# Performance work log

Measured on AMD Instinct MI355X. Metric: run time of the kernel, lower is better.

The kernel has to match this reference:

```python
import jax, jax.numpy as jnp
import numpy as np

N = 100000      # nodes
E = 400000      # edges per relation
R = 4           # relations
D_IN, D_HID, D_OUT = 256, 256, 128


def setup_inputs() -> dict:
    key = jax.random.key(0)
    ks = jax.random.split(key, 6)
    x = jax.random.normal(ks[0], (N, D_IN), jnp.float32)
    src = jax.random.randint(ks[1], (R, E), 0, N)
    dst = jax.random.randint(ks[2], (R, E), 0, N)
    # glorot-ish init for per-relation GraphConv weights
    W1 = jax.random.normal(ks[3], (R, D_IN, D_HID), jnp.float32) * (1.0 / np.sqrt(D_IN))
    b1 = jnp.zeros((R, D_HID), jnp.float32)
    W2 = jax.random.normal(ks[4], (R, D_HID, D_OUT), jnp.float32) * (1.0 / np.sqrt(D_HID))
    b2 = jnp.zeros((R, D_OUT), jnp.float32)
    return {"x": x, "src": src, "dst": dst, "W1": W1, "b1": b1, "W2": W2, "b2": b2}


def _rel_graphconv(x, src, dst, W, b):
    """DGL GraphConv with norm='both': D_dst^{-1/2} A D_src^{-1/2} X W + b.
    x: [N, din]; src/dst: [E]; W: [din, dout]; b: [dout]."""
    n = x.shape[0]
    xw = x @ W                                                   # [N, dout]
    ones = jnp.ones(src.shape, jnp.float32)
    out_deg = jnp.maximum(jax.ops.segment_sum(ones, src, num_segments=n), 1.0)
    in_deg = jnp.maximum(jax.ops.segment_sum(ones, dst, num_segments=n), 1.0)
    msg = xw[src] * (out_deg[src] ** -0.5)[:, None]              # [E, dout] gather + src-norm
    agg = jax.ops.segment_sum(msg, dst, num_segments=n)          # [N, dout] scatter-add
    return agg * (in_deg ** -0.5)[:, None] + b


def _hetero_layer(x, src, dst, W, b):
    # HeteroGraphConv(aggregate='sum'): run GraphConv per relation, sum results.
    conv = jax.vmap(_rel_graphconv, in_axes=(None, 0, 0, 0, 0))
    return jnp.sum(conv(x, src, dst, W, b), axis=0)              # [N, dout]


def reference(x, src, dst, W1, b1, W2, b2):
    h = jax.nn.relu(_hetero_layer(x, src, dst, W1, b1))
    return _hetero_layer(h, src, dst, W2, b2)
```

## Files before the change

### kernel.cpp

```cpp
#include <hip/hip_runtime.h>


#define RELS 4
#define DIN 256
#define DHID 256
#define DOUT 128

typedef short short8 __attribute__((ext_vector_type(8)));
typedef unsigned short ushort8 __attribute__((ext_vector_type(8)));
typedef float f32x4 __attribute__((ext_vector_type(4)));


__device__ __forceinline__ unsigned short f2bf(float f) {
    unsigned int u = __float_as_uint(f);
    u += 0x7FFFu + ((u >> 16) & 1u);
    return (unsigned short)(u >> 16);
}
__device__ __forceinline__ float bf2f(unsigned short u) {
    return __uint_as_float(((unsigned int)u) << 16);
}


__global__ void hist_kernel(const int* __restrict__ src, const int* __restrict__ dst,
                            int* __restrict__ cnt_src, int* __restrict__ cnt_dst,
                            int E, int N) {
    int i = blockIdx.x * blockDim.x + threadIdx.x;
    if (i >= RELS * E) return;
    int r = i / E;
    atomicAdd(cnt_src + (size_t)r * N + src[i], 1);
    atomicAdd(cnt_dst + (size_t)r * N + dst[i], 1);
}

__global__ void norm_kernel(const int* __restrict__ cnt, float* __restrict__ nrm, long n) {
    long i = blockIdx.x * (long)blockDim.x + threadIdx.x;
    if (i >= n) return;
    nrm[i] = rsqrtf(fmaxf((float)cnt[i], 1.0f));
}

__global__ void scan_block(const int* __restrict__ counts, int* __restrict__ out,
                           int* __restrict__ blk_sums, int n) {
    __shared__ int sh[256];
    int i = blockIdx.x * 256 + threadIdx.x;
    int v = (i < n) ? counts[i] : 0;
    sh[threadIdx.x] = v;
    __syncthreads();
#pragma unroll
    for (int off = 1; off < 256; off <<= 1) {
        int t = (threadIdx.x >= off) ? sh[threadIdx.x - off] : 0;
        __syncthreads();
        sh[threadIdx.x] += t;
        __syncthreads();
    }
    if (i < n) out[i] = sh[threadIdx.x] - v;
    if (threadIdx.x == 255) blk_sums[blockIdx.x] = sh[255];
}

__global__ void scan_sums(int* __restrict__ bs, int nb) {
    __shared__ int sh[256];
    __shared__ int carry;
    if (threadIdx.x == 0) carry = 0;
    __syncthreads();
    for (int base = 0; base < nb; base += 256) {
        int i = base + threadIdx.x;
        int v = (i < nb) ? bs[i] : 0;
        sh[threadIdx.x] = v;
        __syncthreads();
#pragma unroll
        for (int off = 1; off < 256; off <<= 1) {
            int t = (threadIdx.x >= off) ? sh[threadIdx.x - off] : 0;
            __syncthreads();
            sh[threadIdx.x] += t;
            __syncthreads();
        }
        if (i < nb) bs[i] = sh[threadIdx.x] - v + carry;
        int tot = sh[255];
        __syncthreads();
        if (threadIdx.x == 255) carry += tot;
        __syncthreads();
    }
}

__global__ void scan_add(int* __restrict__ out, int* __restrict__ cursor,
                         const int* __restrict__ blk_sums, int n, int total) {
    int i = blockIdx.x * 256 + threadIdx.x;
    if (i < n) {
        int v = out[i] + blk_sums[blockIdx.x];
        out[i] = v;
        cursor[i] = v;
    }
    if (i == n - 1) out[n] = total;
}

__global__ void fill_kernel(const int* __restrict__ src, const int* __restrict__ dst,
                            const float* __restrict__ nsrc,
                            int* __restrict__ cursor, int2* __restrict__ e_pack,
                            int E, int N) {
    int i = blockIdx.x * blockDim.x + threadIdx.x;
    if (i >= RELS * E) return;
    int r = i / E;
    int s = src[i];
    int pos = atomicAdd(cursor + (size_t)r * N + dst[i], 1);
    e_pack[pos] = make_int2(s, __float_as_int(nsrc[(size_t)r * N + s]));
}


__global__ void prep_fused(const float* __restrict__ x, const float* __restrict__ W1,
                           const float* __restrict__ W2, const float* __restrict__ b1,
                           const float* __restrict__ b2,
                           unsigned short* __restrict__ x_bf, unsigned short* __restrict__ w1t,
                           unsigned short* __restrict__ w2t,
                           float* __restrict__ b1s, float* __restrict__ b2s, long n8x) {
    const int T1 = RELS * DIN * DHID;
    const int T2 = RELS * DHID * DOUT;
    long i = blockIdx.x * (long)blockDim.x + threadIdx.x;
    if (i < n8x) {
        const float4* ip = (const float4*)(x + i * 8);
        float4 v0 = ip[0], v1 = ip[1];
        ushort4 o0 = make_ushort4(f2bf(v0.x), f2bf(v0.y), f2bf(v0.z), f2bf(v0.w));
        ushort4 o1 = make_ushort4(f2bf(v1.x), f2bf(v1.y), f2bf(v1.z), f2bf(v1.w));
        ushort4* op = (ushort4*)(x_bf + i * 8);
        op[0] = o0; op[1] = o1;
    } else if (i < n8x + T1) {
        int j = (int)(i - n8x);
        int r = j / (DIN * DHID);
        int rem = j - r * (DIN * DHID);
        int k = rem / DHID, n = rem - k * DHID;
        w1t[(size_t)n * (RELS * DIN) + r * DIN + k] = f2bf(W1[j]);
    } else if (i < n8x + T1 + T2) {
        int j = (int)(i - n8x - T1);
        int r = j / (DHID * DOUT);
        int rem = j - r * (DHID * DOUT);
        int k = rem / DOUT, n = rem - k * DOUT;
        w2t[((size_t)r * DOUT + n) * DHID + k] = f2bf(W2[j]);
    } else if (i < n8x + T1 + T2 + DHID + DOUT) {
        int c = (int)(i - n8x - T1 - T2);
        if (c < DHID) {
            b1s[c] = b1[c] + b1[DHID + c] + b1[2 * DHID + c] + b1[3 * DHID + c];
        } else {
            int cc = c - DHID;
            b2s[cc] = b2[cc] + b2[DOUT + cc] + b2[2 * DOUT + cc] + b2[3 * DOUT + cc];
        }
    }
}


__device__ __forceinline__ void gload_lds16(const void* g, void* l) {
    __builtin_amdgcn_global_load_lds(
        (const __attribute__((address_space(1))) void*)g,
        (__attribute__((address_space(3))) void*)l, 16, 0, 0);
}

template <int MODE>
__global__ __launch_bounds__(256) void gemm_bf16(
    const unsigned short* __restrict__ A, const unsigned short* __restrict__ Bt,
    unsigned short* __restrict__ C, int M, int Nout, int K,
    const float* __restrict__ scale_or_bias, int cols_per_rel, int Nnodes) {
    __shared__ unsigned short smA[128 * 32];
    __shared__ unsigned short smB[128 * 32];
    const int tid = threadIdx.x;
    const int lane = tid & 63;
    const int wid = tid >> 6;
    const int wr = wid >> 1, wc = wid & 1;
    const int brow = blockIdx.x * 128, bcol = blockIdx.y * 128;

    f32x4 acc[4][4] = {};

    const int s = lane >> 4;
    const int rl = lane & 15;

    for (int k0 = 0; k0 < K; k0 += 32) {
#pragma unroll
        for (int q = 0; q < 2; ++q) {
            int c = q * 256 + tid;
            int cl = c ^ ((c >> 3) & 3);
            int row = cl >> 2, slot = cl & 3;
            int ga = brow + row; ga = ga < M ? ga : M - 1;
            size_t ldsoff = (size_t)(q * 256 + (tid & ~63)) * 16;
            gload_lds16(A + (size_t)ga * K + k0 + slot * 8, (char*)smA + ldsoff);
            gload_lds16(Bt + (size_t)(bcol + row) * K + k0 + slot * 8, (char*)smB + ldsoff);
        }
        asm volatile("s_waitcnt vmcnt(0)" ::: "memory");
        __syncthreads();

        short8 a[4], b[4];
#pragma unroll
        for (int i = 0; i < 4; ++i) {
            int r = wr * 64 + i * 16 + rl;
            int ch = r * 4 + (s ^ ((r >> 1) & 3));
            a[i] = *(const short8*)((const char*)smA + ch * 16);
        }
#pragma unroll
        for (int j = 0; j < 4; ++j) {
            int r = wc * 64 + j * 16 + rl;
            int ch = r * 4 + (s ^ ((r >> 1) & 3));
            b[j] = *(const short8*)((const char*)smB + ch * 16);
        }
#pragma unroll
        for (int i = 0; i < 4; ++i)
#pragma unroll
            for (int j = 0; j < 4; ++j)
                acc[i][j] = __builtin_amdgcn_mfma_f32_16x16x32_bf16(a[i], b[j], acc[i][j], 0, 0, 0);
        __syncthreads();
    }

    const int rq = lane >> 4;
    if (MODE == 0) {
        const int relid = bcol / cols_per_rel;
        const float* nsr = scale_or_bias + (size_t)relid * Nnodes;
#pragma unroll
        for (int i = 0; i < 4; ++i) {
            int rbase = brow + wr * 64 + i * 16 + rq * 4;
            float sc[4];
#pragma unroll
            for (int t = 0; t < 4; ++t) {
                int row = rbase + t;
                sc[t] = (row < M) ? nsr[row] : 0.f;
            }
#pragma unroll
            for (int j = 0; j < 4; ++j) {
                int col = bcol + wc * 64 + j * 16 + rl;
#pragma unroll
                for (int t = 0; t < 4; ++t) {
                    int row = rbase + t;
                    if (row < M) C[(size_t)row * Nout + col] = f2bf(acc[i][j][t] * sc[t]);
                }
            }
        }
    } else {
#pragma unroll
        for (int i = 0; i < 4; ++i) {
            int rbase = brow + wr * 64 + i * 16 + rq * 4;
#pragma unroll
            for (int j = 0; j < 4; ++j) {
                int col = bcol + wc * 64 + j * 16 + rl;
                float bb = scale_or_bias[col];
#pragma unroll
                for (int t = 0; t < 4; ++t) {
                    int row = rbase + t;
                    if (row < M) C[(size_t)row * Nout + col] = f2bf(fmaxf(acc[i][j][t] + bb, 0.f));
                }
            }
        }
    }
}


__global__ void gather1_agg(const unsigned short* __restrict__ x_bf,
                            const int* __restrict__ rp, const int2* __restrict__ e_pack,
                            const float* __restrict__ ndst,
                            unsigned short* __restrict__ agg4, int N) {
    long w = (blockIdx.x * (long)blockDim.x + threadIdx.x) >> 6;
    int d = (int)(w >> 2);
    if (d >= N) return;
    int r = (int)(w & 3);
    int lane = threadIdx.x & 63;
    int h = lane >> 5, l = lane & 31;
    int beg = rp[(size_t)r * N + d], end = rp[(size_t)r * N + d + 1];
    float acc0[8] = {}, acc1[8] = {};
    int e = beg + h;
    for (; e + 2 < end; e += 4) {
        int2 p0 = e_pack[e];
        int2 p1 = e_pack[e + 2];
        ushort8 v0 = *(const ushort8*)(x_bf + (size_t)p0.x * DIN + l * 8);
        ushort8 v1 = *(const ushort8*)(x_bf + (size_t)p1.x * DIN + l * 8);
        float ns0 = __int_as_float(p0.y);
        float ns1 = __int_as_float(p1.y);
#pragma unroll
        for (int j = 0; j < 8; ++j) {
            acc0[j] += ns0 * bf2f(v0[j]);
            acc1[j] += ns1 * bf2f(v1[j]);
        }
    }
    if (e < end) {
        int2 p0 = e_pack[e];
        ushort8 v0 = *(const ushort8*)(x_bf + (size_t)p0.x * DIN + l * 8);
        float ns0 = __int_as_float(p0.y);
#pragma unroll
        for (int j = 0; j < 8; ++j) acc0[j] += ns0 * bf2f(v0[j]);
    }
    float nd = ndst[(size_t)r * N + d];
    ushort8 o;
#pragma unroll
    for (int j = 0; j < 8; ++j) {
        float v = acc0[j] + acc1[j];
        v += __shfl_xor(v, 32);
        o[j] = f2bf(nd * v);
    }
    if (h == 0)
        __builtin_nontemporal_store(o, (ushort8*)(agg4 + (size_t)d * (RELS * DIN) + r * DIN + l * 8));
}

__global__ void gather2_fused(const unsigned short* __restrict__ hw4,
                              const int* __restrict__ rp, const int2* __restrict__ e_pack,
                              const float* __restrict__ ndst, const float* __restrict__ b2s,
                              float* __restrict__ out, int N) {
    int wid = (int)((blockIdx.x * (long)blockDim.x + threadIdx.x) >> 6);
    if (wid >= N) return;
    int lane = threadIdx.x & 63;
    int h = lane >> 5, l = lane & 31;
    float oacc[4] = {};
#pragma unroll
    for (int r = 0; r < RELS; ++r) {
        int beg = rp[(size_t)r * N + wid], end = rp[(size_t)r * N + wid + 1];
        float acc0[4] = {}, acc1[4] = {};
        int e = beg + h;
        for (; e + 2 < end; e += 4) {
            int s0 = e_pack[e].x;
            int s1 = e_pack[e + 2].x;
            ushort4 v0 = *(const ushort4*)(hw4 + (size_t)s0 * (RELS * DOUT) + r * DOUT + l * 4);
            ushort4 v1 = *(const ushort4*)(hw4 + (size_t)s1 * (RELS * DOUT) + r * DOUT + l * 4);
            acc0[0] += bf2f(v0.x); acc0[1] += bf2f(v0.y); acc0[2] += bf2f(v0.z); acc0[3] += bf2f(v0.w);
            acc1[0] += bf2f(v1.x); acc1[1] += bf2f(v1.y); acc1[2] += bf2f(v1.z); acc1[3] += bf2f(v1.w);
        }
        if (e < end) {
            int s0 = e_pack[e].x;
            ushort4 v0 = *(const ushort4*)(hw4 + (size_t)s0 * (RELS * DOUT) + r * DOUT + l * 4);
            acc0[0] += bf2f(v0.x); acc0[1] += bf2f(v0.y); acc0[2] += bf2f(v0.z); acc0[3] += bf2f(v0.w);
        }
        float nd = ndst[(size_t)r * N + wid];
#pragma unroll
        for (int j = 0; j < 4; ++j) oacc[j] += nd * (acc0[j] + acc1[j]);
    }
#pragma unroll
    for (int j = 0; j < 4; ++j) oacc[j] += __shfl_xor(oacc[j], 32);
    if (h == 0) {
        f32x4 o;
        o[0] = oacc[0] + b2s[l * 4 + 0];
        o[1] = oacc[1] + b2s[l * 4 + 1];
        o[2] = oacc[2] + b2s[l * 4 + 2];
        o[3] = oacc[3] + b2s[l * 4 + 3];
        __builtin_nontemporal_store(o, (f32x4*)(out + (size_t)wid * DOUT + l * 4));
    }
}


extern "C" void kernel_launch(void* const* d_in, const int* in_sizes, int n_in,
                              void* d_out, int out_size, void* d_ws, size_t ws_size,
                              hipStream_t stream) {
    const float* x   = (const float*)d_in[0];
    const int*   src = (const int*)d_in[1];
    const int*   dst = (const int*)d_in[2];
    const float* W1  = (const float*)d_in[3];
    const float* b1  = (const float*)d_in[4];
    const float* W2  = (const float*)d_in[5];
    const float* b2  = (const float*)d_in[6];
    float* out = (float*)d_out;

    const int N = in_sizes[0] / DIN;
    const int E = in_sizes[1] / RELS;
    const int RN = RELS * N;

    char* p = (char*)d_ws;
    int*   cnt_src = (int*)p;    p += (size_t)RN * sizeof(int);
    int*   cnt_dst = (int*)p;    p += (size_t)RN * sizeof(int);
    float* nsrc    = (float*)p;  p += (size_t)RN * sizeof(float);
    float* ndst    = (float*)p;  p += (size_t)RN * sizeof(float);
    int*   row_ptr = (int*)p;    p += ((size_t)RN + 16) * sizeof(int);
    int*   cursor  = (int*)p;    p += (size_t)RN * sizeof(int);
    int2*  e_pack  = (int2*)p;   p += (size_t)RELS * E * sizeof(int2);
    int*   blk_sums= (int*)p;    p += 2048 * sizeof(int);
    float* b1s     = (float*)p;  p += DHID * sizeof(float);
    float* b2s     = (float*)p;  p += DOUT * sizeof(float);
    unsigned short* x_bf = (unsigned short*)p; p += (size_t)N * DIN * sizeof(short);
    unsigned short* w1t  = (unsigned short*)p; p += (size_t)RELS * DIN * DHID * sizeof(short);
    unsigned short* w2t  = (unsigned short*)p; p += (size_t)RELS * DHID * DOUT * sizeof(short);
    unsigned short* h_bf = (unsigned short*)p; p += (size_t)N * DHID * sizeof(short);
    unsigned short* agg4 = (unsigned short*)p; p += (size_t)N * RELS * DIN * sizeof(short);
    unsigned short* hw4  = agg4;

    {
        long n8x = (long)N * DIN / 8;
        long tot = n8x + RELS * DIN * DHID + RELS * DHID * DOUT + DHID + DOUT;
        prep_fused<<<(int)((tot + 255) / 256), 256, 0, stream>>>(
            x, W1, W2, b1, b2, x_bf, w1t, w2t, b1s, b2s, n8x);
    }

    hipMemsetAsync(cnt_src, 0, (size_t)2 * RN * sizeof(int), stream);
    {
        int total = RELS * E;
        hist_kernel<<<(total + 255) / 256, 256, 0, stream>>>(src, dst, cnt_src, cnt_dst, E, N);
        long ntot = (long)2 * RN;
        norm_kernel<<<(int)((ntot + 255) / 256), 256, 0, stream>>>(cnt_src, nsrc, ntot);
    }

    const int nscan = (RN + 255) / 256;
    scan_block<<<nscan, 256, 0, stream>>>(cnt_dst, row_ptr, blk_sums, RN);
    scan_sums<<<1, 256, 0, stream>>>(blk_sums, nscan);
    scan_add<<<nscan, 256, 0, stream>>>(row_ptr, cursor, blk_sums, RN, RELS * E);
    {
        int total = RELS * E;
        fill_kernel<<<(total + 255) / 256, 256, 0, stream>>>(
            src, dst, nsrc, cursor, e_pack, E, N);
    }

    const int gx = (N + 127) / 128;

    {
        long waves = (long)RELS * N;
        int blocks = (int)((waves + 3) / 4);
        gather1_agg<<<blocks, 256, 0, stream>>>(x_bf, row_ptr, e_pack, ndst, agg4, N);
        dim3 grid(gx, DHID / 128);
        gemm_bf16<1><<<grid, 256, 0, stream>>>(agg4, w1t, h_bf, N, DHID, RELS * DIN, b1s, 0, N);
    }

    {
        dim3 grid(gx, (RELS * DOUT) / 128);
        gemm_bf16<0><<<grid, 256, 0, stream>>>(h_bf, w2t, hw4, N, RELS * DOUT, DHID, nsrc, DOUT, N);
        int gblocks = (N + 3) / 4;
        gather2_fused<<<gblocks, 256, 0, stream>>>(hw4, row_ptr, e_pack, ndst, b2s, out, N);
    }
}
```

Baseline: 778.9 us.

## Merge preprocessing launches and replace fill atomics with histogram ranks

Fuses the histogram and the bf16/weight preparation into one launch, and the block scan and degree normalization into another, which cuts the number of kernel launches. The histogram now records each edge's atomic rank within its destination bucket, so the CSR fill computes positions as row_ptr plus rank instead of doing a second round of atomics on a cursor array. The cost is an extra rank array of E*R ints to write and read, plus 64-bit packed edge records written with nontemporal stores.

```diff
diff --git a/kernel.cpp b/kernel.cpp
--- a/kernel.cpp
+++ b/kernel.cpp
@@ -21,38 +21,80 @@
 }
 
 
-__global__ void hist_kernel(const int* __restrict__ src, const int* __restrict__ dst,
-                            int* __restrict__ cnt_src, int* __restrict__ cnt_dst,
-                            int E, int N) {
-    int i = blockIdx.x * blockDim.x + threadIdx.x;
-    if (i >= RELS * E) return;
-    int r = i / E;
-    atomicAdd(cnt_src + (size_t)r * N + src[i], 1);
-    atomicAdd(cnt_dst + (size_t)r * N + dst[i], 1);
-}
-
-__global__ void norm_kernel(const int* __restrict__ cnt, float* __restrict__ nrm, long n) {
-    long i = blockIdx.x * (long)blockDim.x + threadIdx.x;
-    if (i >= n) return;
-    nrm[i] = rsqrtf(fmaxf((float)cnt[i], 1.0f));
-}
-
-__global__ void scan_block(const int* __restrict__ counts, int* __restrict__ out,
-                           int* __restrict__ blk_sums, int n) {
-    __shared__ int sh[256];
-    int i = blockIdx.x * 256 + threadIdx.x;
-    int v = (i < n) ? counts[i] : 0;
-    sh[threadIdx.x] = v;
-    __syncthreads();
-#pragma unroll
-    for (int off = 1; off < 256; off <<= 1) {
-        int t = (threadIdx.x >= off) ? sh[threadIdx.x - off] : 0;
-        __syncthreads();
-        sh[threadIdx.x] += t;
-        __syncthreads();
-    }
-    if (i < n) out[i] = sh[threadIdx.x] - v;
-    if (threadIdx.x == 255) blk_sums[blockIdx.x] = sh[255];
+__global__ void hist_prep(const int* __restrict__ src, const int* __restrict__ dst,
+                          int* __restrict__ cnt_src, int* __restrict__ cnt_dst,
+                          int* __restrict__ rank, int E, int N, int HB,
+                          const float* __restrict__ x, const float* __restrict__ W1,
+                          const float* __restrict__ W2, const float* __restrict__ b1,
+                          const float* __restrict__ b2,
+                          unsigned short* __restrict__ x_bf, unsigned short* __restrict__ w1t,
+                          unsigned short* __restrict__ w2t,
+                          float* __restrict__ b1s, float* __restrict__ b2s, long n8x) {
+    const int T1 = RELS * DIN * DHID;
+    const int T2 = RELS * DHID * DOUT;
+    if ((int)blockIdx.x < HB) {
+        int i = blockIdx.x * 256 + threadIdx.x;
+        if (i >= RELS * E) return;
+        int r = i / E;
+        atomicAdd(cnt_src + (size_t)r * N + src[i], 1);
+        int rk = atomicAdd(cnt_dst + (size_t)r * N + dst[i], 1);
+        __builtin_nontemporal_store(rk, rank + i);
+    } else {
+        long i = (long)(blockIdx.x - HB) * 256 + threadIdx.x;
+        if (i < n8x) {
+            const float4* ip = (const float4*)(x + i * 8);
+            float4 v0 = ip[0], v1 = ip[1];
+            ushort4 o0 = make_ushort4(f2bf(v0.x), f2bf(v0.y), f2bf(v0.z), f2bf(v0.w));
+            ushort4 o1 = make_ushort4(f2bf(v1.x), f2bf(v1.y), f2bf(v1.z), f2bf(v1.w));
+            ushort4* op = (ushort4*)(x_bf + i * 8);
+            op[0] = o0; op[1] = o1;
+        } else if (i < n8x + T1) {
+            int j = (int)(i - n8x);
+            int r = j / (DIN * DHID);
+            int rem = j - r * (DIN * DHID);
+            int k = rem / DHID, n = rem - k * DHID;
+            w1t[(size_t)n * (RELS * DIN) + r * DIN + k] = f2bf(W1[j]);
+        } else if (i < n8x + T1 + T2) {
+            int j = (int)(i - n8x - T1);
+            int r = j / (DHID * DOUT);
+            int rem = j - r * (DHID * DOUT);
+            int k = rem / DOUT, n = rem - k * DOUT;
+            w2t[((size_t)r * DOUT + n) * DHID + k] = f2bf(W2[j]);
+        } else if (i < n8x + T1 + T2 + DHID + DOUT) {
+            int c = (int)(i - n8x - T1 - T2);
+            if (c < DHID) {
+                b1s[c] = b1[c] + b1[DHID + c] + b1[2 * DHID + c] + b1[3 * DHID + c];
+            } else {
+                int cc = c - DHID;
+                b2s[cc] = b2[cc] + b2[DOUT + cc] + b2[2 * DOUT + cc] + b2[3 * DOUT + cc];
+            }
+        }
+    }
+}
+
+
+__global__ void scan_norm(const int* __restrict__ counts, int* __restrict__ out,
+                          int* __restrict__ blk_sums, int n, int SB,
+                          const int* __restrict__ cnt, float* __restrict__ nrm, long nnorm) {
+    if ((int)blockIdx.x < SB) {
+        __shared__ int sh[256];
+        int i = blockIdx.x * 256 + threadIdx.x;
+        int v = (i < n) ? counts[i] : 0;
+        sh[threadIdx.x] = v;
+        __syncthreads();
+#pragma unroll
+        for (int off = 1; off < 256; off <<= 1) {
+            int t = (threadIdx.x >= off) ? sh[threadIdx.x - off] : 0;
+            __syncthreads();
+            sh[threadIdx.x] += t;
+            __syncthreads();
+        }
+        if (i < n) out[i] = sh[threadIdx.x] - v;
+        if (threadIdx.x == 255) blk_sums[blockIdx.x] = sh[255];
+    } else {
+        long i = (long)(blockIdx.x - SB) * 256 + threadIdx.x;
+        if (i < nnorm) nrm[i] = rsqrtf(fmaxf((float)cnt[i], 1.0f));
+    }
 }
 
 __global__ void scan_sums(int* __restrict__ bs, int nb) {
@@ -80,67 +122,26 @@
     }
 }
 
-__global__ void scan_add(int* __restrict__ out, int* __restrict__ cursor,
-                         const int* __restrict__ blk_sums, int n, int total) {
+__global__ void scan_add(int* __restrict__ out, const int* __restrict__ blk_sums,
+                         int n, int total) {
     int i = blockIdx.x * 256 + threadIdx.x;
-    if (i < n) {
-        int v = out[i] + blk_sums[blockIdx.x];
-        out[i] = v;
-        cursor[i] = v;
-    }
+    if (i < n) out[i] += blk_sums[blockIdx.x];
     if (i == n - 1) out[n] = total;
 }
 
+
 __global__ void fill_kernel(const int* __restrict__ src, const int* __restrict__ dst,
-                            const float* __restrict__ nsrc,
-                            int* __restrict__ cursor, int2* __restrict__ e_pack,
+                            const float* __restrict__ nsrc, const int* __restrict__ row_ptr,
+                            const int* __restrict__ rank, long long* __restrict__ e_pack,
                             int E, int N) {
     int i = blockIdx.x * blockDim.x + threadIdx.x;
     if (i >= RELS * E) return;
     int r = i / E;
     int s = src[i];
-    int pos = atomicAdd(cursor + (size_t)r * N + dst[i], 1);
-    e_pack[pos] = make_int2(s, __float_as_int(nsrc[(size_t)r * N + s]));
-}
-
-
-__global__ void prep_fused(const float* __restrict__ x, const float* __restrict__ W1,
-                           const float* __restrict__ W2, const float* __restrict__ b1,
-                           const float* __restrict__ b2,
-                           unsigned short* __restrict__ x_bf, unsigned short* __restrict__ w1t,
-                           unsigned short* __restrict__ w2t,
-                           float* __restrict__ b1s, float* __restrict__ b2s, long n8x) {
-    const int T1 = RELS * DIN * DHID;
-    const int T2 = RELS * DHID * DOUT;
-    long i = blockIdx.x * (long)blockDim.x + threadIdx.x;
-    if (i < n8x) {
-        const float4* ip = (const float4*)(x + i * 8);
-        float4 v0 = ip[0], v1 = ip[1];
-        ushort4 o0 = make_ushort4(f2bf(v0.x), f2bf(v0.y), f2bf(v0.z), f2bf(v0.w));
-        ushort4 o1 = make_ushort4(f2bf(v1.x), f2bf(v1.y), f2bf(v1.z), f2bf(v1.w));
-        ushort4* op = (ushort4*)(x_bf + i * 8);
-        op[0] = o0; op[1] = o1;
-    } else if (i < n8x + T1) {
-        int j = (int)(i - n8x);
-        int r = j / (DIN * DHID);
-        int rem = j - r * (DIN * DHID);
-        int k = rem / DHID, n = rem - k * DHID;
-        w1t[(size_t)n * (RELS * DIN) + r * DIN + k] = f2bf(W1[j]);
-    } else if (i < n8x + T1 + T2) {
-        int j = (int)(i - n8x - T1);
-        int r = j / (DHID * DOUT);
-        int rem = j - r * (DHID * DOUT);
-        int k = rem / DOUT, n = rem - k * DOUT;
-        w2t[((size_t)r * DOUT + n) * DHID + k] = f2bf(W2[j]);
-    } else if (i < n8x + T1 + T2 + DHID + DOUT) {
-        int c = (int)(i - n8x - T1 - T2);
-        if (c < DHID) {
-            b1s[c] = b1[c] + b1[DHID + c] + b1[2 * DHID + c] + b1[3 * DHID + c];
-        } else {
-            int cc = c - DHID;
-            b2s[cc] = b2[cc] + b2[DOUT + cc] + b2[2 * DOUT + cc] + b2[3 * DOUT + cc];
-        }
-    }
+    int pos = row_ptr[(size_t)r * N + dst[i]] + rank[i];
+    unsigned long long v = (unsigned int)s |
+        ((unsigned long long)(unsigned int)__float_as_int(nsrc[(size_t)r * N + s]) << 32);
+    __builtin_nontemporal_store((long long)v, e_pack + pos);
 }
 
 
@@ -246,7 +247,7 @@
 
 
 __global__ void gather1_agg(const unsigned short* __restrict__ x_bf,
-                            const int* __restrict__ rp, const int2* __restrict__ e_pack,
+                            const int* __restrict__ rp, const long long* __restrict__ e_pack,
                             const float* __restrict__ ndst,
                             unsigned short* __restrict__ agg4, int N) {
     long w = (blockIdx.x * (long)blockDim.x + threadIdx.x) >> 6;
@@ -259,12 +260,14 @@
     float acc0[8] = {}, acc1[8] = {};
     int e = beg + h;
     for (; e + 2 < end; e += 4) {
-        int2 p0 = e_pack[e];
-        int2 p1 = e_pack[e + 2];
-        ushort8 v0 = *(const ushort8*)(x_bf + (size_t)p0.x * DIN + l * 8);
-        ushort8 v1 = *(const ushort8*)(x_bf + (size_t)p1.x * DIN + l * 8);
-        float ns0 = __int_as_float(p0.y);
-        float ns1 = __int_as_float(p1.y);
+        unsigned long long p0 = (unsigned long long)e_pack[e];
+        unsigned long long p1 = (unsigned long long)e_pack[e + 2];
+        int s0 = (int)(unsigned int)p0;
+        int s1 = (int)(unsigned int)p1;
+        ushort8 v0 = *(const ushort8*)(x_bf + (size_t)s0 * DIN + l * 8);
+        ushort8 v1 = *(const ushort8*)(x_bf + (size_t)s1 * DIN + l * 8);
+        float ns0 = __uint_as_float((unsigned int)(p0 >> 32));
+        float ns1 = __uint_as_float((unsigned int)(p1 >> 32));
 #pragma unroll
         for (int j = 0; j < 8; ++j) {
             acc0[j] += ns0 * bf2f(v0[j]);
@@ -272,9 +275,10 @@
         }
     }
     if (e < end) {
-        int2 p0 = e_pack[e];
-        ushort8 v0 = *(const ushort8*)(x_bf + (size_t)p0.x * DIN + l * 8);
-        float ns0 = __int_as_float(p0.y);
+        unsigned long long p0 = (unsigned long long)e_pack[e];
+        int s0 = (int)(unsigned int)p0;
+        ushort8 v0 = *(const ushort8*)(x_bf + (size_t)s0 * DIN + l * 8);
+        float ns0 = __uint_as_float((unsigned int)(p0 >> 32));
 #pragma unroll
         for (int j = 0; j < 8; ++j) acc0[j] += ns0 * bf2f(v0[j]);
     }
@@ -291,7 +295,7 @@
 }
 
 __global__ void gather2_fused(const unsigned short* __restrict__ hw4,
-                              const int* __restrict__ rp, const int2* __restrict__ e_pack,
+                              const int* __restrict__ rp, const long long* __restrict__ e_pack,
                               const float* __restrict__ ndst, const float* __restrict__ b2s,
                               float* __restrict__ out, int N) {
     int wid = (int)((blockIdx.x * (long)blockDim.x + threadIdx.x) >> 6);
@@ -305,15 +309,15 @@
         float acc0[4] = {}, acc1[4] = {};
         int e = beg + h;
         for (; e + 2 < end; e += 4) {
-            int s0 = e_pack[e].x;
-            int s1 = e_pack[e + 2].x;
+            int s0 = (int)(unsigned int)(unsigned long long)e_pack[e];
+            int s1 = (int)(unsigned int)(unsigned long long)e_pack[e + 2];
             ushort4 v0 = *(const ushort4*)(hw4 + (size_t)s0 * (RELS * DOUT) + r * DOUT + l * 4);
             ushort4 v1 = *(const ushort4*)(hw4 + (size_t)s1 * (RELS * DOUT) + r * DOUT + l * 4);
             acc0[0] += bf2f(v0.x); acc0[1] += bf2f(v0.y); acc0[2] += bf2f(v0.z); acc0[3] += bf2f(v0.w);
             acc1[0] += bf2f(v1.x); acc1[1] += bf2f(v1.y); acc1[2] += bf2f(v1.z); acc1[3] += bf2f(v1.w);
         }
         if (e < end) {
-            int s0 = e_pack[e].x;
+            int s0 = (int)(unsigned int)(unsigned long long)e_pack[e];
             ushort4 v0 = *(const ushort4*)(hw4 + (size_t)s0 * (RELS * DOUT) + r * DOUT + l * 4);
             acc0[0] += bf2f(v0.x); acc0[1] += bf2f(v0.y); acc0[2] += bf2f(v0.z); acc0[3] += bf2f(v0.w);
         }
@@ -356,8 +360,8 @@
     float* nsrc    = (float*)p;  p += (size_t)RN * sizeof(float);
     float* ndst    = (float*)p;  p += (size_t)RN * sizeof(float);
     int*   row_ptr = (int*)p;    p += ((size_t)RN + 16) * sizeof(int);
-    int*   cursor  = (int*)p;    p += (size_t)RN * sizeof(int);
-    int2*  e_pack  = (int2*)p;   p += (size_t)RELS * E * sizeof(int2);
+    int*   rank    = (int*)p;    p += (size_t)RELS * E * sizeof(int);
+    long long* e_pack = (long long*)p; p += (size_t)RELS * E * sizeof(long long);
     int*   blk_sums= (int*)p;    p += 2048 * sizeof(int);
     float* b1s     = (float*)p;  p += DHID * sizeof(float);
     float* b2s     = (float*)p;  p += DOUT * sizeof(float);
@@ -368,29 +372,31 @@
     unsigned short* agg4 = (unsigned short*)p; p += (size_t)N * RELS * DIN * sizeof(short);
     unsigned short* hw4  = agg4;
 
+    hipMemsetAsync(cnt_src, 0, (size_t)2 * RN * sizeof(int), stream);
+    const long n8x = (long)N * DIN / 8;
     {
-        long n8x = (long)N * DIN / 8;
-        long tot = n8x + RELS * DIN * DHID + RELS * DHID * DOUT + DHID + DOUT;
-        prep_fused<<<(int)((tot + 255) / 256), 256, 0, stream>>>(
+        const int HB = (RELS * E + 255) / 256;
+        long preptot = n8x + RELS * DIN * DHID + RELS * DHID * DOUT + DHID + DOUT;
+        int PB = (int)((preptot + 255) / 256);
+        hist_prep<<<HB + PB, 256, 0, stream>>>(
+            src, dst, cnt_src, cnt_dst, rank, E, N, HB,
             x, W1, W2, b1, b2, x_bf, w1t, w2t, b1s, b2s, n8x);
     }
 
-    hipMemsetAsync(cnt_src, 0, (size_t)2 * RN * sizeof(int), stream);
+    const int nscan = (RN + 255) / 256;
     {
-        int total = RELS * E;
-        hist_kernel<<<(total + 255) / 256, 256, 0, stream>>>(src, dst, cnt_src, cnt_dst, E, N);
-        long ntot = (long)2 * RN;
-        norm_kernel<<<(int)((ntot + 255) / 256), 256, 0, stream>>>(cnt_src, nsrc, ntot);
-    }
-
-    const int nscan = (RN + 255) / 256;
-    scan_block<<<nscan, 256, 0, stream>>>(cnt_dst, row_ptr, blk_sums, RN);
+        long nnorm = (long)2 * RN;
+        int NB = (int)((nnorm + 255) / 256);
+        scan_norm<<<nscan + NB, 256, 0, stream>>>(
+            cnt_dst, row_ptr, blk_sums, RN, nscan, cnt_src, nsrc, nnorm);
+    }
     scan_sums<<<1, 256, 0, stream>>>(blk_sums, nscan);
-    scan_add<<<nscan, 256, 0, stream>>>(row_ptr, cursor, blk_sums, RN, RELS * E);
+    scan_add<<<nscan, 256, 0, stream>>>(row_ptr, blk_sums, RN, RELS * E);
+
     {
         int total = RELS * E;
         fill_kernel<<<(total + 255) / 256, 256, 0, stream>>>(
-            src, dst, nsrc, cursor, e_pack, E, N);
+            src, dst, nsrc, row_ptr, rank, e_pack, E, N);
     }
 
     const int gx = (N + 127) / 128;
```

Result: slower. 803.9 us (+3.2%).
